# Performance work log

Measured on AMD Instinct MI355X. Metric: run time of the kernel, lower is better.

The kernel has to match this reference:

```python
import jax, jax.numpy as jnp
import numpy as np
from jax import lax

B, H, W, C = 2, 96, 96, 96
D_STATE, D_CONV, EXPAND = 16, 3, 2
D_INNER = EXPAND * C            # 192 (VSSBlock inner width)
DM = D_INNER                    # Mamba d_model; Mamba expand=1 -> mamba d_inner == DM
DT_RANK = -(-DM // 16)          # ceil(192/16) = 12


def setup_inputs() -> dict:
    key = jax.random.key(0)
    ks = jax.random.split(key, 12)
    s = lambda k, shp, sc=0.02: jax.random.normal(k, shp, jnp.float32) * sc
    return {
        "x": jax.random.normal(ks[0], (B, H, W, C), jnp.float32),
        "norm_w": jnp.ones((C,), jnp.float32),
        "norm_b": jnp.zeros((C,), jnp.float32),
        "in_proj_w": s(ks[1], (C, 2 * D_INNER)),
        "conv2d_w": s(ks[2], (D_INNER, 1, D_CONV, D_CONV), 0.1),   # depthwise OIHW
        "m_in_proj_w": s(ks[3], (DM, 2 * DM)),
        "m_conv1d_w": s(ks[4], (DM, 1, D_CONV), 0.1),              # depthwise causal OIL
        "m_conv1d_b": jnp.zeros((DM,), jnp.float32),
        "m_x_proj_w": s(ks[5], (DM, DT_RANK + 2 * D_STATE)),
        "m_dt_proj_w": s(ks[6], (DT_RANK, DM), 0.1),
        "m_dt_proj_b": s(ks[7], (DM,), 0.1),
        "m_A_log": jnp.log(jnp.broadcast_to(
            jnp.arange(1, D_STATE + 1, dtype=jnp.float32), (DM, D_STATE))),
        "m_D": jnp.ones((DM,), jnp.float32),
        "m_out_proj_w": s(ks[8], (DM, DM)),
        "out_proj_w": s(ks[9], (D_INNER, C)),
    }


def _layernorm(x, w, b, eps=1e-5):
    mu = x.mean(-1, keepdims=True)
    var = jnp.mean(jnp.square(x - mu), -1, keepdims=True)
    return (x - mu) * lax.rsqrt(var + eps) * w + b


def _selective_scan(u, delta, A, Bm, Cm, Dv):
    # u, delta: (B,L,D); A: (D,N); Bm, Cm: (B,L,N); Dv: (D,)
    dA = jnp.exp(jnp.einsum('bld,dn->bldn', delta, A))           # (B,L,D,N)
    dBu = jnp.einsum('bld,bln->bldn', delta * u, Bm)             # (B,L,D,N)

    def step(h, inp):
        dA_t, dBu_t, C_t = inp
        h = dA_t * h + dBu_t                                      # (B,D,N)
        y = jnp.einsum('bdn,bn->bd', h, C_t)
        return h, y

    h0 = jnp.zeros((u.shape[0], A.shape[0], A.shape[1]), u.dtype)
    xs = (dA.transpose(1, 0, 2, 3), dBu.transpose(1, 0, 2, 3), Cm.transpose(1, 0, 2))
    _, ys = lax.scan(step, h0, xs)
    return ys.transpose(1, 0, 2) + u * Dv                         # (B,L,D)


def _mamba(seq, m_in_proj_w, m_conv1d_w, m_conv1d_b, m_x_proj_w,
           m_dt_proj_w, m_dt_proj_b, m_A_log, m_D, m_out_proj_w):
    # seq: (B,L,DM)
    xm, z = jnp.split(seq @ m_in_proj_w, 2, axis=-1)
    # causal depthwise conv1d over L
    xc = lax.conv_general_dilated(
        jnp.transpose(xm, (0, 2, 1)), m_conv1d_w, (1,), [(D_CONV - 1, 0)],
        feature_group_count=DM, dimension_numbers=('NCH', 'OIH', 'NCH'))
    xm = jax.nn.silu(jnp.transpose(xc + m_conv1d_b[None, :, None], (0, 2, 1)))
    x_dbl = xm @ m_x_proj_w
    dt, Bm, Cm = jnp.split(x_dbl, [DT_RANK, DT_RANK + D_STATE], axis=-1)
    delta = jax.nn.softplus(dt @ m_dt_proj_w + m_dt_proj_b)
    A = -jnp.exp(m_A_log)
    y = _selective_scan(xm, delta, A, Bm, Cm, m_D)
    return (y * jax.nn.silu(z)) @ m_out_proj_w


def reference(x, norm_w, norm_b, in_proj_w, conv2d_w, m_in_proj_w, m_conv1d_w,
              m_conv1d_b, m_x_proj_w, m_dt_proj_w, m_dt_proj_b, m_A_log, m_D,
              m_out_proj_w, out_proj_w):
    Bsz, Hh, Ww, _ = x.shape
    xn = _layernorm(x, norm_w, norm_b)
    x_in, x_gate = jnp.split(xn @ in_proj_w, 2, axis=-1)          # (B,H,W,D_INNER) x2
    # depthwise 3x3 conv, 'same' padding
    xc = lax.conv_general_dilated(
        jnp.transpose(x_in, (0, 3, 1, 2)), conv2d_w, (1, 1), [(1, 1), (1, 1)],
        feature_group_count=D_INNER, dimension_numbers=('NCHW', 'OIHW', 'NCHW'))
    xc = jax.nn.silu(jnp.transpose(xc, (0, 2, 3, 1)))
    seq = xc.reshape(Bsz, Hh * Ww, D_INNER)
    y = _mamba(seq, m_in_proj_w, m_conv1d_w, m_conv1d_b, m_x_proj_w,
               m_dt_proj_w, m_dt_proj_b, m_A_log, m_D, m_out_proj_w)
    y = y.reshape(Bsz, Hh, Ww, D_INNER) * jax.nn.silu(x_gate)
    return x + y @ out_proj_w
```

## Files before the change

kernel.cpp:

```cpp
#include <hip/hip_runtime.h>

#define DEV_INLINE __device__ __forceinline__

constexpr int BATCH = 2;
constexpr int HH = 96, WW = 96, CC = 96;
constexpr int DI = 192;
constexpr int NS = 16;
constexpr int LSEQ = HH * WW;
constexpr int TT = BATCH * LSEQ;
constexpr int CHUNK = 32;
constexpr int NCHUNK = LSEQ / CHUNK;
constexpr int SUP = 24;
constexpr int NSUP = NCHUNK / SUP;
constexpr int QDN = DI * NS;

typedef __attribute__((ext_vector_type(8))) short bf16x8;
typedef __attribute__((ext_vector_type(4))) float f32x4;

DEV_INLINE float silu_f(float x) { return x / (1.f + __expf(-x)); }
DEV_INLINE float softplus_f(float x) {
  return fmaxf(x, 0.f) + log1pf(__expf(-fabsf(x)));
}
DEV_INLINE ushort f2bf(float f) {
  union { float f; unsigned u; } c; c.f = f;
  unsigned u = c.u + 0x7FFF + ((c.u >> 16) & 1);
  return (ushort)(u >> 16);
}

__global__ __launch_bounds__(256)
void castw_kernel(const float* __restrict__ w0, const float* __restrict__ w1,
                  const float* __restrict__ w2, const float* __restrict__ w3,
                  ushort* __restrict__ t0, ushort* __restrict__ t1,
                  ushort* __restrict__ t2, ushort* __restrict__ t3)
{
  int id = blockIdx.x * 256 + threadIdx.x;
  if (id < 36864) {
    int k = id % 96, n = id / 96;
    t0[id] = f2bf(w0[k * 384 + n]);
  } else if (id < 110592) {
    int j = id - 36864; int k = j % 192, n = j / 192;
    t1[j] = f2bf(w1[k * 384 + n]);
  } else if (id < 147456) {
    int j = id - 110592; int k = j % 192, n = j / 192;
    t2[j] = f2bf(w2[k * 192 + n]);
  } else {
    int j = id - 147456; int k = j % 192, n = j / 192;
    t3[j] = (n < 96) ? f2bf(w3[k * 96 + n]) : (ushort)0;
  }
}

__global__ __launch_bounds__(256)
void ln_kernel(const float* __restrict__ x, const float* __restrict__ w,
               const float* __restrict__ bb, ushort* __restrict__ xn)
{
  int wid = (blockIdx.x * blockDim.x + threadIdx.x) >> 6;
  int lane = threadIdx.x & 63;
  if (wid >= TT) return;
  const float* xr = x + (size_t)wid * CC;
  float v0 = xr[lane];
  float v1 = (lane < 32) ? xr[64 + lane] : 0.f;
  float s = v0 + v1, ss = v0 * v0 + v1 * v1;
#pragma unroll
  for (int off = 32; off >= 1; off >>= 1) {
    s  += __shfl_xor(s, off);
    ss += __shfl_xor(ss, off);
  }
  float mean = s * (1.f / 96.f);
  float var  = ss * (1.f / 96.f) - mean * mean;
  float rstd = rsqrtf(var + 1e-5f);
  ushort* o = xn + (size_t)wid * CC;
  o[lane] = f2bf((v0 - mean) * rstd * w[lane] + bb[lane]);
  if (lane < 32) o[64 + lane] = f2bf((v1 - mean) * rstd * w[64 + lane] + bb[64 + lane]);
}

template<int EPI, int OUTF>
__global__ __launch_bounds__(256)
void mfma_gemm_kernel(const ushort* __restrict__ A, int lda,
                      const ushort* __restrict__ Bt, int ldb,
                      void* __restrict__ Cout, int ldc, int N, int K,
                      const float* __restrict__ aux, int ldaux)
{
  const int tid = threadIdx.x;
  const int wid = tid >> 6, lane = tid & 63;
  const int wm = wid >> 1, wn = wid & 1;
  const int m0 = blockIdx.x * 128 + wm * 64;
  const int n0 = blockIdx.y * 64 + wn * 32;
  const int row16 = lane & 15, quad = lane >> 4;

  f32x4 acc[4][2];
  const f32x4 z4 = {0.f, 0.f, 0.f, 0.f};
#pragma unroll
  for (int i = 0; i < 4; ++i)
#pragma unroll
    for (int j = 0; j < 2; ++j) acc[i][j] = z4;

  for (int k0 = 0; k0 < K; k0 += 32) {
    bf16x8 a[4], b[2];
#pragma unroll
    for (int i = 0; i < 4; ++i)
      a[i] = *(const bf16x8*)(A + (size_t)(m0 + i * 16 + row16) * lda + k0 + quad * 8);
#pragma unroll
    for (int j = 0; j < 2; ++j)
      b[j] = *(const bf16x8*)(Bt + (size_t)(n0 + j * 16 + row16) * ldb + k0 + quad * 8);
#pragma unroll
    for (int i = 0; i < 4; ++i)
#pragma unroll
      for (int j = 0; j < 2; ++j)
        acc[i][j] = __builtin_amdgcn_mfma_f32_16x16x32_bf16(a[i], b[j], acc[i][j], 0, 0, 0);
  }

#pragma unroll
  for (int i = 0; i < 4; ++i) {
    const int rowb = m0 + i * 16 + quad * 4;
#pragma unroll
    for (int j = 0; j < 2; ++j) {
      const int col = n0 + j * 16 + row16;
      if (col < N) {
#pragma unroll
        for (int r = 0; r < 4; ++r) {
          float v = acc[i][j][r];
          const int row = rowb + r;
          if (EPI == 1) v *= silu_f(aux[(size_t)row * ldaux + col]);
          else if (EPI == 2) v += aux[(size_t)row * ldaux + col];
          if (OUTF == 0) ((float*)Cout)[(size_t)row * ldc + col] = v;
          else ((ushort*)Cout)[(size_t)row * ldc + col] = f2bf(v);
        }
      }
    }
  }
}

__global__ __launch_bounds__(256)
void gemm_f32_kernel(const float* __restrict__ A, int lda,
                     const float* __restrict__ B, int ldb,
                     float* __restrict__ C, int ldc, int N, int K)
{
  __shared__ __align__(16) float As[16][132];
  __shared__ __align__(16) float Bs[16][64];
  const int tid = threadIdx.x;
  const int tx = tid & 15;
  const int ty = tid >> 4;
  const int m0 = blockIdx.x * 128;
  const int n0 = blockIdx.y * 64;
  const int arow = tid >> 2;
  const int akq  = (tid & 3) << 2;
  const int brow = tid >> 4;
  const int bcol = (tid & 15) << 2;

  float acc[8][4];
#pragma unroll
  for (int i = 0; i < 8; ++i)
#pragma unroll
    for (int j = 0; j < 4; ++j) acc[i][j] = 0.f;

  for (int k0 = 0; k0 < K; k0 += 16) {
    float4 a0 = *(const float4*)(A + (size_t)(m0 + arow) * lda + (k0 + akq));
    float4 a1 = *(const float4*)(A + (size_t)(m0 + arow + 64) * lda + (k0 + akq));
    float4 bv = make_float4(0.f, 0.f, 0.f, 0.f);
    if (n0 + bcol < N)
      bv = *(const float4*)(B + (size_t)(k0 + brow) * ldb + (n0 + bcol));
    __syncthreads();
    As[akq + 0][arow] = a0.x;
    As[akq + 1][arow] = a0.y;
    As[akq + 2][arow] = a0.z;
    As[akq + 3][arow] = a0.w;
    As[akq + 0][arow + 64] = a1.x;
    As[akq + 1][arow + 64] = a1.y;
    As[akq + 2][arow + 64] = a1.z;
    As[akq + 3][arow + 64] = a1.w;
    *(float4*)&Bs[brow][bcol] = bv;
    __syncthreads();
#pragma unroll
    for (int k = 0; k < 16; ++k) {
      float4 av0 = *(const float4*)&As[k][ty * 8];
      float4 av1 = *(const float4*)&As[k][ty * 8 + 4];
      float4 bv0 = *(const float4*)&Bs[k][tx * 4];
      float am[8] = {av0.x, av0.y, av0.z, av0.w, av1.x, av1.y, av1.z, av1.w};
      float bn[4] = {bv0.x, bv0.y, bv0.z, bv0.w};
#pragma unroll
      for (int i = 0; i < 8; ++i)
#pragma unroll
        for (int j = 0; j < 4; ++j)
          acc[i][j] = fmaf(am[i], bn[j], acc[i][j]);
    }
  }

  const int col = n0 + tx * 4;
  if (col < N) {
#pragma unroll
    for (int i = 0; i < 8; ++i) {
      const int row = m0 + ty * 8 + i;
      *(float4*)(C + (size_t)row * ldc + col) =
          make_float4(acc[i][0], acc[i][1], acc[i][2], acc[i][3]);
    }
  }
}

__global__ __launch_bounds__(256)
void conv2d_silu_kernel(const float* __restrict__ xz0, const float* __restrict__ w,
                        ushort* __restrict__ xc)
{
  __shared__ float ws[DI * 9];
  for (int i = threadIdx.x; i < DI * 9; i += 256) ws[i] = w[i];
  __syncthreads();
  int id = blockIdx.x * 256 + threadIdx.x;
  int dq = id % 48;
  int p  = id / 48;
  int j = p % WW;
  int i = (p / WW) % HH;
  int b = p / (WW * HH);
  int d = dq * 4;
  float a0 = 0.f, a1 = 0.f, a2 = 0.f, a3 = 0.f;
#pragma unroll
  for (int ki = 0; ki < 3; ++ki) {
    int ii = i + ki - 1;
    if (ii < 0 || ii >= HH) continue;
#pragma unroll
    for (int kj = 0; kj < 3; ++kj) {
      int jj = j + kj - 1;
      if (jj < 0 || jj >= WW) continue;
      const float4 v = *(const float4*)(xz0 + ((size_t)((b * HH + ii) * WW + jj)) * 384 + d);
      int wk = ki * 3 + kj;
      a0 = fmaf(v.x, ws[(d + 0) * 9 + wk], a0);
      a1 = fmaf(v.y, ws[(d + 1) * 9 + wk], a1);
      a2 = fmaf(v.z, ws[(d + 2) * 9 + wk], a2);
      a3 = fmaf(v.w, ws[(d + 3) * 9 + wk], a3);
    }
  }
  ushort4 o;
  o.x = f2bf(silu_f(a0)); o.y = f2bf(silu_f(a1));
  o.z = f2bf(silu_f(a2)); o.w = f2bf(silu_f(a3));
  *(ushort4*)(xc + (size_t)p * DI + d) = o;
}

__global__ __launch_bounds__(256)
void conv1d_silu_kernel(const float* __restrict__ xz1, const float* __restrict__ w,
                        const float* __restrict__ bias, float* __restrict__ xm)
{
  int id = blockIdx.x * 256 + threadIdx.x;
  int dq = id % 48;
  int t  = id / 48;
  int l  = t % LSEQ;
  int d  = dq * 4;
  float a0 = bias[d + 0], a1 = bias[d + 1], a2 = bias[d + 2], a3 = bias[d + 3];
#pragma unroll
  for (int k = 0; k < 3; ++k) {
    int ll = l + k - 2;
    if (ll < 0) continue;
    const float4 v = *(const float4*)(xz1 + (size_t)(t + k - 2) * 384 + d);
    a0 = fmaf(v.x, w[(d + 0) * 3 + k], a0);
    a1 = fmaf(v.y, w[(d + 1) * 3 + k], a1);
    a2 = fmaf(v.z, w[(d + 2) * 3 + k], a2);
    a3 = fmaf(v.w, w[(d + 3) * 3 + k], a3);
  }
  float4 o = make_float4(silu_f(a0), silu_f(a1), silu_f(a2), silu_f(a3));
  *(float4*)(xm + (size_t)t * DI + d) = o;
}

__global__ __launch_bounds__(256)
void dtproj_kernel(const float* __restrict__ xdbl, const float* __restrict__ Wdt,
                   const float* __restrict__ bdt, float* __restrict__ delta)
{
  int id = blockIdx.x * 256 + threadIdx.x;
  int d = id % DI;
  int t = id / DI;
  float acc = bdt[d];
#pragma unroll
  for (int r = 0; r < 12; ++r)
    acc = fmaf(xdbl[(size_t)t * 44 + r], Wdt[r * DI + d], acc);
  delta[id] = softplus_f(acc);
}

__global__ __launch_bounds__(192)
void scan1_kernel(const float* __restrict__ dlt, const float* __restrict__ xmb,
                  const float* __restrict__ xdbl, const float* __restrict__ Alog,
                  float* __restrict__ P, float* __restrict__ E)
{
  const int d = threadIdx.x;
  const int g = blockIdx.x % NCHUNK;
  const int b = blockIdx.x / NCHUNK;
  const int t0 = b * LSEQ + g * CHUNK;
  float Av[16];
#pragma unroll
  for (int j = 0; j < 16; ++j) Av[j] = -__expf(Alog[d * 16 + j]);
  float e[16];
#pragma unroll
  for (int j = 0; j < 16; ++j) e[j] = 0.f;
  float sdl = 0.f;
#pragma unroll 2
  for (int l = 0; l < CHUNK; ++l) {
    const int t = t0 + l;
    float dl = dlt[(size_t)t * DI + d];
    float u  = xmb[(size_t)t * DI + d];
    const float4 B0 = *(const float4*)(xdbl + (size_t)t * 44 + 12);
    const float4 B1 = *(const float4*)(xdbl + (size_t)t * 44 + 16);
    const float4 B2 = *(const float4*)(xdbl + (size_t)t * 44 + 20);
    const float4 B3 = *(const float4*)(xdbl + (size_t)t * 44 + 24);
    const float Bv[16] = {B0.x, B0.y, B0.z, B0.w, B1.x, B1.y, B1.z, B1.w,
                          B2.x, B2.y, B2.z, B2.w, B3.x, B3.y, B3.z, B3.w};
    float du = dl * u;
    sdl += dl;
#pragma unroll
    for (int j = 0; j < 16; ++j) {
      float a = __expf(dl * Av[j]);
      e[j] = fmaf(a, e[j], du * Bv[j]);
    }
  }
  size_t base = ((size_t)(b * NCHUNK + g)) * QDN + d * 16;
#pragma unroll
  for (int j = 0; j < 16; ++j) {
    P[base + j] = __expf(Av[j] * sdl);
    E[base + j] = e[j];
  }
}

__global__ __launch_bounds__(256)
void scan2a_kernel(const float* __restrict__ P, const float* __restrict__ E,
                   float* __restrict__ SP, float* __restrict__ SE)
{
  int id = blockIdx.x * 256 + threadIdx.x;
  int q = id % QDN;
  int s = (id / QDN) % NSUP;
  int b = id / (QDN * NSUP);
  float cp = 1.f, ce = 0.f;
#pragma unroll 4
  for (int c = 0; c < SUP; ++c) {
    size_t idx = ((size_t)(b * NCHUNK + s * SUP + c)) * QDN + q;
    float p = P[idx], e = E[idx];
    ce = fmaf(p, ce, e);
    cp *= p;
  }
  SP[id] = cp; SE[id] = ce;
}

__global__ __launch_bounds__(256)
void scan2b_kernel(const float* __restrict__ SP, const float* __restrict__ SE,
                   float* __restrict__ Hsup)
{
  int id = blockIdx.x * 256 + threadIdx.x;
  int q = id % QDN;
  int b = id / QDN;
  float carry = 0.f;
#pragma unroll
  for (int s = 0; s < NSUP; ++s) {
    size_t idx = ((size_t)(b * NSUP + s)) * QDN + q;
    Hsup[idx] = carry;
    carry = fmaf(SP[idx], carry, SE[idx]);
  }
}

__global__ __launch_bounds__(256)
void scan2c_kernel(const float* __restrict__ P, const float* __restrict__ E,
                   const float* __restrict__ Hsup, float* __restrict__ Hin)
{
  int id = blockIdx.x * 256 + threadIdx.x;
  int q = id % QDN;
  int s = (id / QDN) % NSUP;
  int b = id / (QDN * NSUP);
  float h = Hsup[id];
#pragma unroll 4
  for (int c = 0; c < SUP; ++c) {
    size_t idx = ((size_t)(b * NCHUNK + s * SUP + c)) * QDN + q;
    Hin[idx] = h;
    h = fmaf(P[idx], h, E[idx]);
  }
}

__global__ __launch_bounds__(192)
void scan3_kernel(const float* __restrict__ dlt, const float* __restrict__ xmb,
                  const float* __restrict__ xdbl, const float* __restrict__ Alog,
                  const float* __restrict__ Dv, const float* __restrict__ xz1,
                  const float* __restrict__ Hin, ushort* __restrict__ yout)
{
  const int d = threadIdx.x;
  const int g = blockIdx.x % NCHUNK;
  const int b = blockIdx.x / NCHUNK;
  const int t0 = b * LSEQ + g * CHUNK;
  float Av[16];
#pragma unroll
  for (int j = 0; j < 16; ++j) Av[j] = -__expf(Alog[d * 16 + j]);
  const float Dd = Dv[d];
  float h[16];
  {
    size_t hb = ((size_t)(b * NCHUNK + g)) * QDN + d * 16;
#pragma unroll
    for (int j = 0; j < 16; ++j) h[j] = Hin[hb + j];
  }
#pragma unroll 2
  for (int l = 0; l < CHUNK; ++l) {
    const int t = t0 + l;
    float dl = dlt[(size_t)t * DI + d];
    float u  = xmb[(size_t)t * DI + d];
    const float4 B0 = *(const float4*)(xdbl + (size_t)t * 44 + 12);
    const float4 B1 = *(const float4*)(xdbl + (size_t)t * 44 + 16);
    const float4 B2 = *(const float4*)(xdbl + (size_t)t * 44 + 20);
    const float4 B3 = *(const float4*)(xdbl + (size_t)t * 44 + 24);
    const float4 C0 = *(const float4*)(xdbl + (size_t)t * 44 + 28);
    const float4 C1 = *(const float4*)(xdbl + (size_t)t * 44 + 32);
    const float4 C2 = *(const float4*)(xdbl + (size_t)t * 44 + 36);
    const float4 C3 = *(const float4*)(xdbl + (size_t)t * 44 + 40);
    const float Bv[16] = {B0.x, B0.y, B0.z, B0.w, B1.x, B1.y, B1.z, B1.w,
                          B2.x, B2.y, B2.z, B2.w, B3.x, B3.y, B3.z, B3.w};
    const float Cv[16] = {C0.x, C0.y, C0.z, C0.w, C1.x, C1.y, C1.z, C1.w,
                          C2.x, C2.y, C2.z, C2.w, C3.x, C3.y, C3.z, C3.w};
    float du = dl * u;
    float y0 = 0.f, y1 = 0.f, y2 = 0.f, y3 = 0.f;
#pragma unroll
    for (int j = 0; j < 16; ++j) {
      float a = __expf(dl * Av[j]);
      h[j] = fmaf(a, h[j], du * Bv[j]);
      if ((j & 3) == 0) y0 = fmaf(h[j], Cv[j], y0);
      else if ((j & 3) == 1) y1 = fmaf(h[j], Cv[j], y1);
      else if ((j & 3) == 2) y2 = fmaf(h[j], Cv[j], y2);
      else y3 = fmaf(h[j], Cv[j], y3);
    }
    float y = (y0 + y1) + (y2 + y3) + u * Dd;
    float z = xz1[(size_t)t * 384 + 192 + d];
    yout[(size_t)t * DI + d] = f2bf(y * silu_f(z));
  }
}

extern "C" void kernel_launch(void* const* d_in, const int* in_sizes, int n_in,
                              void* d_out, int out_size, void* d_ws, size_t ws_size,
                              hipStream_t stream)
{
  const float* x         = (const float*)d_in[0];
  const float* norm_w    = (const float*)d_in[1];
  const float* norm_b    = (const float*)d_in[2];
  const float* in_proj_w = (const float*)d_in[3];
  const float* conv2d_w  = (const float*)d_in[4];
  const float* m_in_proj = (const float*)d_in[5];
  const float* m_c1d_w   = (const float*)d_in[6];
  const float* m_c1d_b   = (const float*)d_in[7];
  const float* m_x_proj  = (const float*)d_in[8];
  const float* m_dt_w    = (const float*)d_in[9];
  const float* m_dt_b    = (const float*)d_in[10];
  const float* m_A_log   = (const float*)d_in[11];
  const float* m_D       = (const float*)d_in[12];
  const float* m_out_w   = (const float*)d_in[13];
  const float* out_w     = (const float*)d_in[14];
  float* out = (float*)d_out;

  char* wp = (char*)d_ws;
  auto alloc = [&](size_t bytes) {
    char* r = wp; wp += (bytes + 255) & ~(size_t)255; return r;
  };
  ushort* Wt0   = (ushort*)alloc(36864 * 2);
  ushort* Wt1   = (ushort*)alloc(73728 * 2);
  ushort* Wt2   = (ushort*)alloc(36864 * 2);
  ushort* Wt3   = (ushort*)alloc(24576 * 2);
  ushort* xn_bf = (ushort*)alloc((size_t)TT * 96 * 2);
  float*  xz0   = (float*)alloc((size_t)TT * 384 * 4);
  ushort* xc_bf = (ushort*)alloc((size_t)TT * 192 * 2);
  float*  xz1   = (float*)alloc((size_t)TT * 384 * 4);
  float*  xmb   = (float*)alloc((size_t)TT * 192 * 4);
  float*  xdbl  = (float*)alloc((size_t)TT * 44 * 4);
  float*  dlt   = (float*)alloc((size_t)TT * 192 * 4);
  float*  Pb    = (float*)alloc((size_t)BATCH * NCHUNK * QDN * 4);
  float*  Eb    = (float*)alloc((size_t)BATCH * NCHUNK * QDN * 4);
  float*  Hin   = (float*)alloc((size_t)BATCH * NCHUNK * QDN * 4);
  float*  SPb   = (float*)alloc((size_t)BATCH * NSUP * QDN * 4);
  float*  SEb   = (float*)alloc((size_t)BATCH * NSUP * QDN * 4);
  float*  Hsup  = (float*)alloc((size_t)BATCH * NSUP * QDN * 4);
  ushort* yfin  = (ushort*)alloc((size_t)TT * 192 * 2);
  ushort* yg    = (ushort*)alloc((size_t)TT * 192 * 2);

  castw_kernel<<<672, 256, 0, stream>>>(in_proj_w, m_in_proj, m_out_w, out_w,
                                        Wt0, Wt1, Wt2, Wt3);
  ln_kernel<<<TT / 4, 256, 0, stream>>>(x, norm_w, norm_b, xn_bf);
  mfma_gemm_kernel<0, 0><<<dim3(TT / 128, 6), 256, 0, stream>>>(
      xn_bf, 96, Wt0, 96, xz0, 384, 384, 96, nullptr, 0);
  conv2d_silu_kernel<<<TT * 48 / 256, 256, 0, stream>>>(xz0, conv2d_w, xc_bf);
  mfma_gemm_kernel<0, 0><<<dim3(TT / 128, 6), 256, 0, stream>>>(
      xc_bf, 192, Wt1, 192, xz1, 384, 384, 192, nullptr, 0);
  conv1d_silu_kernel<<<TT * 48 / 256, 256, 0, stream>>>(xz1, m_c1d_w, m_c1d_b, xmb);
  gemm_f32_kernel<<<dim3(TT / 128, 1), 256, 0, stream>>>(xmb, 192, m_x_proj, 44, xdbl, 44, 44, 192);
  dtproj_kernel<<<TT * 192 / 256, 256, 0, stream>>>(xdbl, m_dt_w, m_dt_b, dlt);
  scan1_kernel<<<BATCH * NCHUNK, 192, 0, stream>>>(dlt, xmb, xdbl, m_A_log, Pb, Eb);
  scan2a_kernel<<<BATCH * NSUP * QDN / 256, 256, 0, stream>>>(Pb, Eb, SPb, SEb);
  scan2b_kernel<<<BATCH * QDN / 256, 256, 0, stream>>>(SPb, SEb, Hsup);
  scan2c_kernel<<<BATCH * NSUP * QDN / 256, 256, 0, stream>>>(Pb, Eb, Hsup, Hin);
  scan3_kernel<<<BATCH * NCHUNK, 192, 0, stream>>>(dlt, xmb, xdbl, m_A_log, m_D, xz1, Hin, yfin);
  mfma_gemm_kernel<1, 1><<<dim3(TT / 128, 3), 256, 0, stream>>>(
      yfin, 192, Wt2, 192, yg, 192, 192, 192, xz0 + 192, 384);
  mfma_gemm_kernel<2, 0><<<dim3(TT / 128, 2), 256, 0, stream>>>(
      yg, 192, Wt3, 192, out, 96, 96, 192, x, 96);
}
```

Baseline: 271.0 us.

## Fuse conv1d, x_proj and dt_proj into one MFMA kernel; store intermediates in bf16

Replaces the separate conv1d+silu, fp32 x_proj GEMM and dt_proj kernels with a single mamba_prep kernel. It computes the causal conv into shared memory, then runs x_proj and dt_proj as bf16 MFMA, with B/C reordered into a compact 32-float layout. The in_proj intermediates xz0/xz1 and xm are now stored as bf16. The GEMM epilogue is transposed so each lane writes four contiguous outputs per token. The aim is to cut launches and global memory traffic, at the cost of reduced precision in dt, B and C and in the activations feeding the scan.

Result: no change. 267.6 us (-1.3%).

```diff
diff --git a/kernel.cpp b/kernel.cpp
--- a/kernel.cpp
+++ b/kernel.cpp
@@ -26,12 +26,17 @@
   unsigned u = c.u + 0x7FFF + ((c.u >> 16) & 1);
   return (ushort)(u >> 16);
 }
+DEV_INLINE float bf2f(ushort u) {
+  union { unsigned u; float f; } c; c.u = ((unsigned)u) << 16; return c.f;
+}
 
 __global__ __launch_bounds__(256)
 void castw_kernel(const float* __restrict__ w0, const float* __restrict__ w1,
                   const float* __restrict__ w2, const float* __restrict__ w3,
+                  const float* __restrict__ wx, const float* __restrict__ wdt,
                   ushort* __restrict__ t0, ushort* __restrict__ t1,
-                  ushort* __restrict__ t2, ushort* __restrict__ t3)
+                  ushort* __restrict__ t2, ushort* __restrict__ t3,
+                  ushort* __restrict__ t4, ushort* __restrict__ t5)
 {
   int id = blockIdx.x * 256 + threadIdx.x;
   if (id < 36864) {
@@ -43,9 +48,19 @@
   } else if (id < 147456) {
     int j = id - 110592; int k = j % 192, n = j / 192;
     t2[j] = f2bf(w2[k * 192 + n]);
-  } else {
+  } else if (id < 172032) {
     int j = id - 147456; int k = j % 192, n = j / 192;
     t3[j] = (n < 96) ? f2bf(w3[k * 96 + n]) : (ushort)0;
+  } else if (id < 181248) {
+    int j = id - 172032; int k = j % 192, n = j / 192;
+    float v = 0.f;
+    if (n < 16) v = wx[k * 44 + 12 + n];
+    else if (n < 32) v = wx[k * 44 + 28 + (n - 16)];
+    else if (n < 44) v = wx[k * 44 + (n - 32)];
+    t4[j] = f2bf(v);
+  } else {
+    int j = id - 181248; int r = j % 32, d = j / 32;
+    t5[j] = (r < 12) ? f2bf(wdt[r * 192 + d]) : (ushort)0;
   }
 }
 
@@ -78,14 +93,14 @@
 void mfma_gemm_kernel(const ushort* __restrict__ A, int lda,
                       const ushort* __restrict__ Bt, int ldb,
                       void* __restrict__ Cout, int ldc, int N, int K,
-                      const float* __restrict__ aux, int ldaux)
+                      const void* __restrict__ aux, int ldaux)
 {
   const int tid = threadIdx.x;
   const int wid = tid >> 6, lane = tid & 63;
   const int wm = wid >> 1, wn = wid & 1;
   const int m0 = blockIdx.x * 128 + wm * 64;
   const int n0 = blockIdx.y * 64 + wn * 32;
-  const int row16 = lane & 15, quad = lane >> 4;
+  const int l16 = lane & 15, quad = lane >> 4;
 
   f32x4 acc[4][2];
   const f32x4 z4 = {0.f, 0.f, 0.f, 0.f};
@@ -95,109 +110,52 @@
     for (int j = 0; j < 2; ++j) acc[i][j] = z4;
 
   for (int k0 = 0; k0 < K; k0 += 32) {
-    bf16x8 a[4], b[2];
+    bf16x8 xf[4], wf[2];
 #pragma unroll
     for (int i = 0; i < 4; ++i)
-      a[i] = *(const bf16x8*)(A + (size_t)(m0 + i * 16 + row16) * lda + k0 + quad * 8);
+      xf[i] = *(const bf16x8*)(A + (size_t)(m0 + i * 16 + l16) * lda + k0 + quad * 8);
 #pragma unroll
     for (int j = 0; j < 2; ++j)
-      b[j] = *(const bf16x8*)(Bt + (size_t)(n0 + j * 16 + row16) * ldb + k0 + quad * 8);
+      wf[j] = *(const bf16x8*)(Bt + (size_t)(n0 + j * 16 + l16) * ldb + k0 + quad * 8);
 #pragma unroll
     for (int i = 0; i < 4; ++i)
 #pragma unroll
       for (int j = 0; j < 2; ++j)
-        acc[i][j] = __builtin_amdgcn_mfma_f32_16x16x32_bf16(a[i], b[j], acc[i][j], 0, 0, 0);
+        acc[i][j] = __builtin_amdgcn_mfma_f32_16x16x32_bf16(wf[j], xf[i], acc[i][j], 0, 0, 0);
   }
 
 #pragma unroll
   for (int i = 0; i < 4; ++i) {
-    const int rowb = m0 + i * 16 + quad * 4;
+    const int token = m0 + i * 16 + l16;
 #pragma unroll
     for (int j = 0; j < 2; ++j) {
-      const int col = n0 + j * 16 + row16;
-      if (col < N) {
-#pragma unroll
-        for (int r = 0; r < 4; ++r) {
-          float v = acc[i][j][r];
-          const int row = rowb + r;
-          if (EPI == 1) v *= silu_f(aux[(size_t)row * ldaux + col]);
-          else if (EPI == 2) v += aux[(size_t)row * ldaux + col];
-          if (OUTF == 0) ((float*)Cout)[(size_t)row * ldc + col] = v;
-          else ((ushort*)Cout)[(size_t)row * ldc + col] = f2bf(v);
-        }
+      const int nb = n0 + j * 16 + quad * 4;
+      if (nb >= N) continue;
+      float v[4];
+#pragma unroll
+      for (int r = 0; r < 4; ++r) v[r] = acc[i][j][r];
+      if (EPI == 1) {
+        const ushort4 g4 = *(const ushort4*)((const ushort*)aux + (size_t)token * ldaux + nb);
+        v[0] *= silu_f(bf2f(g4.x)); v[1] *= silu_f(bf2f(g4.y));
+        v[2] *= silu_f(bf2f(g4.z)); v[3] *= silu_f(bf2f(g4.w));
+      } else if (EPI == 2) {
+        const float4 r4 = *(const float4*)((const float*)aux + (size_t)token * ldaux + nb);
+        v[0] += r4.x; v[1] += r4.y; v[2] += r4.z; v[3] += r4.w;
       }
-    }
-  }
-}
-
-__global__ __launch_bounds__(256)
-void gemm_f32_kernel(const float* __restrict__ A, int lda,
-                     const float* __restrict__ B, int ldb,
-                     float* __restrict__ C, int ldc, int N, int K)
-{
-  __shared__ __align__(16) float As[16][132];
-  __shared__ __align__(16) float Bs[16][64];
-  const int tid = threadIdx.x;
-  const int tx = tid & 15;
-  const int ty = tid >> 4;
-  const int m0 = blockIdx.x * 128;
-  const int n0 = blockIdx.y * 64;
-  const int arow = tid >> 2;
-  const int akq  = (tid & 3) << 2;
-  const int brow = tid >> 4;
-  const int bcol = (tid & 15) << 2;
-
-  float acc[8][4];
-#pragma unroll
-  for (int i = 0; i < 8; ++i)
-#pragma unroll
-    for (int j = 0; j < 4; ++j) acc[i][j] = 0.f;
-
-  for (int k0 = 0; k0 < K; k0 += 16) {
-    float4 a0 = *(const float4*)(A + (size_t)(m0 + arow) * lda + (k0 + akq));
-    float4 a1 = *(const float4*)(A + (size_t)(m0 + arow + 64) * lda + (k0 + akq));
-    float4 bv = make_float4(0.f, 0.f, 0.f, 0.f);
-    if (n0 + bcol < N)
-      bv = *(const float4*)(B + (size_t)(k0 + brow) * ldb + (n0 + bcol));
-    __syncthreads();
-    As[akq + 0][arow] = a0.x;
-    As[akq + 1][arow] = a0.y;
-    As[akq + 2][arow] = a0.z;
-    As[akq + 3][arow] = a0.w;
-    As[akq + 0][arow + 64] = a1.x;
-    As[akq + 1][arow + 64] = a1.y;
-    As[akq + 2][arow + 64] = a1.z;
-    As[akq + 3][arow + 64] = a1.w;
-    *(float4*)&Bs[brow][bcol] = bv;
-    __syncthreads();
-#pragma unroll
-    for (int k = 0; k < 16; ++k) {
-      float4 av0 = *(const float4*)&As[k][ty * 8];
-      float4 av1 = *(const float4*)&As[k][ty * 8 + 4];
-      float4 bv0 = *(const float4*)&Bs[k][tx * 4];
-      float am[8] = {av0.x, av0.y, av0.z, av0.w, av1.x, av1.y, av1.z, av1.w};
-      float bn[4] = {bv0.x, bv0.y, bv0.z, bv0.w};
-#pragma unroll
-      for (int i = 0; i < 8; ++i)
-#pragma unroll
-        for (int j = 0; j < 4; ++j)
-          acc[i][j] = fmaf(am[i], bn[j], acc[i][j]);
-    }
-  }
-
-  const int col = n0 + tx * 4;
-  if (col < N) {
-#pragma unroll
-    for (int i = 0; i < 8; ++i) {
-      const int row = m0 + ty * 8 + i;
-      *(float4*)(C + (size_t)row * ldc + col) =
-          make_float4(acc[i][0], acc[i][1], acc[i][2], acc[i][3]);
-    }
-  }
-}
-
-__global__ __launch_bounds__(256)
-void conv2d_silu_kernel(const float* __restrict__ xz0, const float* __restrict__ w,
+      if (OUTF == 0) {
+        *(float4*)((float*)Cout + (size_t)token * ldc + nb) =
+            make_float4(v[0], v[1], v[2], v[3]);
+      } else {
+        ushort4 o;
+        o.x = f2bf(v[0]); o.y = f2bf(v[1]); o.z = f2bf(v[2]); o.w = f2bf(v[3]);
+        *(ushort4*)((ushort*)Cout + (size_t)token * ldc + nb) = o;
+      }
+    }
+  }
+}
+
+__global__ __launch_bounds__(256)
+void conv2d_silu_kernel(const ushort* __restrict__ xz0, const float* __restrict__ w,
                         ushort* __restrict__ xc)
 {
   __shared__ float ws[DI * 9];
@@ -219,12 +177,12 @@
     for (int kj = 0; kj < 3; ++kj) {
       int jj = j + kj - 1;
       if (jj < 0 || jj >= WW) continue;
-      const float4 v = *(const float4*)(xz0 + ((size_t)((b * HH + ii) * WW + jj)) * 384 + d);
+      const ushort4 v = *(const ushort4*)(xz0 + ((size_t)((b * HH + ii) * WW + jj)) * 384 + d);
       int wk = ki * 3 + kj;
-      a0 = fmaf(v.x, ws[(d + 0) * 9 + wk], a0);
-      a1 = fmaf(v.y, ws[(d + 1) * 9 + wk], a1);
-      a2 = fmaf(v.z, ws[(d + 2) * 9 + wk], a2);
-      a3 = fmaf(v.w, ws[(d + 3) * 9 + wk], a3);
+      a0 = fmaf(bf2f(v.x), ws[(d + 0) * 9 + wk], a0);
+      a1 = fmaf(bf2f(v.y), ws[(d + 1) * 9 + wk], a1);
+      a2 = fmaf(bf2f(v.z), ws[(d + 2) * 9 + wk], a2);
+      a3 = fmaf(bf2f(v.w), ws[(d + 3) * 9 + wk], a3);
     }
   }
   ushort4 o;
@@ -234,46 +192,93 @@
 }
 
 __global__ __launch_bounds__(256)
-void conv1d_silu_kernel(const float* __restrict__ xz1, const float* __restrict__ w,
-                        const float* __restrict__ bias, float* __restrict__ xm)
-{
-  int id = blockIdx.x * 256 + threadIdx.x;
-  int dq = id % 48;
-  int t  = id / 48;
-  int l  = t % LSEQ;
-  int d  = dq * 4;
-  float a0 = bias[d + 0], a1 = bias[d + 1], a2 = bias[d + 2], a3 = bias[d + 3];
-#pragma unroll
-  for (int k = 0; k < 3; ++k) {
-    int ll = l + k - 2;
-    if (ll < 0) continue;
-    const float4 v = *(const float4*)(xz1 + (size_t)(t + k - 2) * 384 + d);
-    a0 = fmaf(v.x, w[(d + 0) * 3 + k], a0);
-    a1 = fmaf(v.y, w[(d + 1) * 3 + k], a1);
-    a2 = fmaf(v.z, w[(d + 2) * 3 + k], a2);
-    a3 = fmaf(v.w, w[(d + 3) * 3 + k], a3);
-  }
-  float4 o = make_float4(silu_f(a0), silu_f(a1), silu_f(a2), silu_f(a3));
-  *(float4*)(xm + (size_t)t * DI + d) = o;
-}
-
-__global__ __launch_bounds__(256)
-void dtproj_kernel(const float* __restrict__ xdbl, const float* __restrict__ Wdt,
-                   const float* __restrict__ bdt, float* __restrict__ delta)
-{
-  int id = blockIdx.x * 256 + threadIdx.x;
-  int d = id % DI;
-  int t = id / DI;
-  float acc = bdt[d];
-#pragma unroll
-  for (int r = 0; r < 12; ++r)
-    acc = fmaf(xdbl[(size_t)t * 44 + r], Wdt[r * DI + d], acc);
-  delta[id] = softplus_f(acc);
+void mamba_prep_kernel(const ushort* __restrict__ xz1, const float* __restrict__ cw,
+                       const float* __restrict__ cb, const ushort* __restrict__ Wxt,
+                       const ushort* __restrict__ Wdtt, const float* __restrict__ bdt,
+                       ushort* __restrict__ xmb_bf, float* __restrict__ xdbl_bc,
+                       float* __restrict__ dlt)
+{
+  __shared__ ushort sxm[64][200];
+  __shared__ ushort sdtb[64][40];
+  const int tid = threadIdx.x;
+  const int t0 = blockIdx.x * 64;
+  const int l0 = t0 % LSEQ;
+
+  for (int i = tid; i < 64 * 40 / 2; i += 256) ((unsigned*)sdtb)[i] = 0;
+
+#pragma unroll
+  for (int it = 0; it < 12; ++it) {
+    int task = tid + it * 256;
+    int dq = task % 48, tl = task / 48;
+    int d = dq * 4;
+    int t = t0 + tl, l = l0 + tl;
+    float a0 = cb[d], a1 = cb[d + 1], a2 = cb[d + 2], a3 = cb[d + 3];
+#pragma unroll
+    for (int k = 0; k < 3; ++k) {
+      if (l + k - 2 < 0) continue;
+      const ushort4 v = *(const ushort4*)(xz1 + (size_t)(t + k - 2) * 384 + d);
+      a0 = fmaf(bf2f(v.x), cw[(d + 0) * 3 + k], a0);
+      a1 = fmaf(bf2f(v.y), cw[(d + 1) * 3 + k], a1);
+      a2 = fmaf(bf2f(v.z), cw[(d + 2) * 3 + k], a2);
+      a3 = fmaf(bf2f(v.w), cw[(d + 3) * 3 + k], a3);
+    }
+    ushort4 o;
+    o.x = f2bf(silu_f(a0)); o.y = f2bf(silu_f(a1));
+    o.z = f2bf(silu_f(a2)); o.w = f2bf(silu_f(a3));
+    *(ushort4*)&sxm[tl][d] = o;
+    *(ushort4*)(xmb_bf + (size_t)t * DI + d) = o;
+  }
+  __syncthreads();
+
+  const int wid = tid >> 6, lane = tid & 63;
+  const int l16 = lane & 15, quad = lane >> 4;
+  const int ts = wid * 16;
+  const int token = t0 + ts + l16;
+  const f32x4 z4 = {0.f, 0.f, 0.f, 0.f};
+
+  f32x4 acc1[3] = {z4, z4, z4};
+  for (int k0 = 0; k0 < 192; k0 += 32) {
+    bf16x8 xf = *(const bf16x8*)&sxm[ts + l16][k0 + quad * 8];
+#pragma unroll
+    for (int j = 0; j < 3; ++j) {
+      bf16x8 wf = *(const bf16x8*)(Wxt + (size_t)(j * 16 + l16) * 192 + k0 + quad * 8);
+      acc1[j] = __builtin_amdgcn_mfma_f32_16x16x32_bf16(wf, xf, acc1[j], 0, 0, 0);
+    }
+  }
+#pragma unroll
+  for (int j = 0; j < 2; ++j)
+    *(float4*)(xdbl_bc + (size_t)token * 32 + j * 16 + quad * 4) =
+        make_float4(acc1[j][0], acc1[j][1], acc1[j][2], acc1[j][3]);
+  if (quad < 3) {
+    ushort4 o;
+    o.x = f2bf(acc1[2][0]); o.y = f2bf(acc1[2][1]);
+    o.z = f2bf(acc1[2][2]); o.w = f2bf(acc1[2][3]);
+    *(ushort4*)&sdtb[ts + l16][quad * 4] = o;
+  }
+  __syncthreads();
+
+  bf16x8 dtf = *(const bf16x8*)&sdtb[ts + l16][quad * 8];
+  f32x4 acc2[12];
+#pragma unroll
+  for (int jj = 0; jj < 12; ++jj) {
+    bf16x8 wf = *(const bf16x8*)(Wdtt + (size_t)(jj * 16 + l16) * 32 + quad * 8);
+    acc2[jj] = __builtin_amdgcn_mfma_f32_16x16x32_bf16(wf, dtf, z4, 0, 0, 0);
+  }
+#pragma unroll
+  for (int jj = 0; jj < 12; ++jj) {
+    const int nb = jj * 16 + quad * 4;
+    float4 dv;
+    dv.x = softplus_f(acc2[jj][0] + bdt[nb + 0]);
+    dv.y = softplus_f(acc2[jj][1] + bdt[nb + 1]);
+    dv.z = softplus_f(acc2[jj][2] + bdt[nb + 2]);
+    dv.w = softplus_f(acc2[jj][3] + bdt[nb + 3]);
+    *(float4*)(dlt + (size_t)token * DI + nb) = dv;
+  }
 }
 
 __global__ __launch_bounds__(192)
-void scan1_kernel(const float* __restrict__ dlt, const float* __restrict__ xmb,
-                  const float* __restrict__ xdbl, const float* __restrict__ Alog,
+void scan1_kernel(const float* __restrict__ dlt, const ushort* __restrict__ xmb,
+                  const float* __restrict__ xdbl_bc, const float* __restrict__ Alog,
                   float* __restrict__ P, float* __restrict__ E)
 {
   const int d = threadIdx.x;
@@ -291,11 +296,11 @@
   for (int l = 0; l < CHUNK; ++l) {
     const int t = t0 + l;
     float dl = dlt[(size_t)t * DI + d];
-    float u  = xmb[(size_t)t * DI + d];
-    const float4 B0 = *(const float4*)(xdbl + (size_t)t * 44 + 12);
-    const float4 B1 = *(const float4*)(xdbl + (size_t)t * 44 + 16);
-    const float4 B2 = *(const float4*)(xdbl + (size_t)t * 44 + 20);
-    const float4 B3 = *(const float4*)(xdbl + (size_t)t * 44 + 24);
+    float u  = bf2f(xmb[(size_t)t * DI + d]);
+    const float4 B0 = *(const float4*)(xdbl_bc + (size_t)t * 32 + 0);
+    const float4 B1 = *(const float4*)(xdbl_bc + (size_t)t * 32 + 4);
+    const float4 B2 = *(const float4*)(xdbl_bc + (size_t)t * 32 + 8);
+    const float4 B3 = *(const float4*)(xdbl_bc + (size_t)t * 32 + 12);
     const float Bv[16] = {B0.x, B0.y, B0.z, B0.w, B1.x, B1.y, B1.z, B1.w,
                           B2.x, B2.y, B2.z, B2.w, B3.x, B3.y, B3.z, B3.w};
     float du = dl * u;
@@ -367,9 +372,9 @@
 }
 
 __global__ __launch_bounds__(192)
-void scan3_kernel(const float* __restrict__ dlt, const float* __restrict__ xmb,
-                  const float* __restrict__ xdbl, const float* __restrict__ Alog,
-                  const float* __restrict__ Dv, const float* __restrict__ xz1,
+void scan3_kernel(const float* __restrict__ dlt, const ushort* __restrict__ xmb,
+                  const float* __restrict__ xdbl_bc, const float* __restrict__ Alog,
+                  const float* __restrict__ Dv, const ushort* __restrict__ xz1,
                   const float* __restrict__ Hin, ushort* __restrict__ yout)
 {
   const int d = threadIdx.x;
@@ -390,15 +395,15 @@
   for (int l = 0; l < CHUNK; ++l) {
     const int t = t0 + l;
     float dl = dlt[(size_t)t * DI + d];
-    float u  = xmb[(size_t)t * DI + d];
-    const float4 B0 = *(const float4*)(xdbl + (size_t)t * 44 + 12);
-    const float4 B1 = *(const float4*)(xdbl + (size_t)t * 44 + 16);
-    const float4 B2 = *(const float4*)(xdbl + (size_t)t * 44 + 20);
-    const float4 B3 = *(const float4*)(xdbl + (size_t)t * 44 + 24);
-    const float4 C0 = *(const float4*)(xdbl + (size_t)t * 44 + 28);
-    const float4 C1 = *(const float4*)(xdbl + (size_t)t * 44 + 32);
-    const float4 C2 = *(const float4*)(xdbl + (size_t)t * 44 + 36);
-    const float4 C3 = *(const float4*)(xdbl + (size_t)t * 44 + 40);
+    float u  = bf2f(xmb[(size_t)t * DI + d]);
+    const float4 B0 = *(const float4*)(xdbl_bc + (size_t)t * 32 + 0);
+    const float4 B1 = *(const float4*)(xdbl_bc + (size_t)t * 32 + 4);
+    const float4 B2 = *(const float4*)(xdbl_bc + (size_t)t * 32 + 8);
+    const float4 B3 = *(const float4*)(xdbl_bc + (size_t)t * 32 + 12);
+    const float4 C0 = *(const float4*)(xdbl_bc + (size_t)t * 32 + 16);
+    const float4 C1 = *(const float4*)(xdbl_bc + (size_t)t * 32 + 20);
+    const float4 C2 = *(const float4*)(xdbl_bc + (size_t)t * 32 + 24);
+    const float4 C3 = *(const float4*)(xdbl_bc + (size_t)t * 32 + 28);
     const float Bv[16] = {B0.x, B0.y, B0.z, B0.w, B1.x, B1.y, B1.z, B1.w,
                           B2.x, B2.y, B2.z, B2.w, B3.x, B3.y, B3.z, B3.w};
     const float Cv[16] = {C0.x, C0.y, C0.z, C0.w, C1.x, C1.y, C1.z, C1.w,
@@ -415,7 +420,7 @@
       else y3 = fmaf(h[j], Cv[j], y3);
     }
     float y = (y0 + y1) + (y2 + y3) + u * Dd;
-    float z = xz1[(size_t)t * 384 + 192 + d];
+    float z = bf2f(xz1[(size_t)t * 384 + 192 + d]);
     yout[(size_t)t * DI + d] = f2bf(y * silu_f(z));
   }
 }
@@ -445,42 +450,44 @@
   auto alloc = [&](size_t bytes) {
     char* r = wp; wp += (bytes + 255) & ~(size_t)255; return r;
   };
-  ushort* Wt0   = (ushort*)alloc(36864 * 2);
-  ushort* Wt1   = (ushort*)alloc(73728 * 2);
-  ushort* Wt2   = (ushort*)alloc(36864 * 2);
-  ushort* Wt3   = (ushort*)alloc(24576 * 2);
-  ushort* xn_bf = (ushort*)alloc((size_t)TT * 96 * 2);
-  float*  xz0   = (float*)alloc((size_t)TT * 384 * 4);
-  ushort* xc_bf = (ushort*)alloc((size_t)TT * 192 * 2);
-  float*  xz1   = (float*)alloc((size_t)TT * 384 * 4);
-  float*  xmb   = (float*)alloc((size_t)TT * 192 * 4);
-  float*  xdbl  = (float*)alloc((size_t)TT * 44 * 4);
-  float*  dlt   = (float*)alloc((size_t)TT * 192 * 4);
-  float*  Pb    = (float*)alloc((size_t)BATCH * NCHUNK * QDN * 4);
-  float*  Eb    = (float*)alloc((size_t)BATCH * NCHUNK * QDN * 4);
-  float*  Hin   = (float*)alloc((size_t)BATCH * NCHUNK * QDN * 4);
-  float*  SPb   = (float*)alloc((size_t)BATCH * NSUP * QDN * 4);
-  float*  SEb   = (float*)alloc((size_t)BATCH * NSUP * QDN * 4);
-  float*  Hsup  = (float*)alloc((size_t)BATCH * NSUP * QDN * 4);
-  ushort* yfin  = (ushort*)alloc((size_t)TT * 192 * 2);
-  ushort* yg    = (ushort*)alloc((size_t)TT * 192 * 2);
-
-  castw_kernel<<<672, 256, 0, stream>>>(in_proj_w, m_in_proj, m_out_w, out_w,
-                                        Wt0, Wt1, Wt2, Wt3);
+  ushort* Wt0    = (ushort*)alloc(36864 * 2);
+  ushort* Wt1    = (ushort*)alloc(73728 * 2);
+  ushort* Wt2    = (ushort*)alloc(36864 * 2);
+  ushort* Wt3    = (ushort*)alloc(24576 * 2);
+  ushort* Wxt    = (ushort*)alloc(9216 * 2);
+  ushort* Wdtt   = (ushort*)alloc(6144 * 2);
+  ushort* xn_bf  = (ushort*)alloc((size_t)TT * 96 * 2);
+  ushort* xz0    = (ushort*)alloc((size_t)TT * 384 * 2);
+  ushort* xc_bf  = (ushort*)alloc((size_t)TT * 192 * 2);
+  ushort* xz1    = (ushort*)alloc((size_t)TT * 384 * 2);
+  ushort* xmb_bf = (ushort*)alloc((size_t)TT * 192 * 2);
+  float*  xdbl_bc= (float*)alloc((size_t)TT * 32 * 4);
+  float*  dlt    = (float*)alloc((size_t)TT * 192 * 4);
+  float*  Pb     = (float*)alloc((size_t)BATCH * NCHUNK * QDN * 4);
+  float*  Eb     = (float*)alloc((size_t)BATCH * NCHUNK * QDN * 4);
+  float*  Hin    = (float*)alloc((size_t)BATCH * NCHUNK * QDN * 4);
+  float*  SPb    = (float*)alloc((size_t)BATCH * NSUP * QDN * 4);
+  float*  SEb    = (float*)alloc((size_t)BATCH * NSUP * QDN * 4);
+  float*  Hsup   = (float*)alloc((size_t)BATCH * NSUP * QDN * 4);
+  ushort* yfin   = (ushort*)alloc((size_t)TT * 192 * 2);
+  ushort* yg     = (ushort*)alloc((size_t)TT * 192 * 2);
+
+  castw_kernel<<<732, 256, 0, stream>>>(in_proj_w, m_in_proj, m_out_w, out_w,
+                                        m_x_proj, m_dt_w,
+                                        Wt0, Wt1, Wt2, Wt3, Wxt, Wdtt);
   ln_kernel<<<TT / 4, 256, 0, stream>>>(x, norm_w, norm_b, xn_bf);
-  mfma_gemm_kernel<0, 0><<<dim3(TT / 128, 6), 256, 0, stream>>>(
+  mfma_gemm_kernel<0, 1><<<dim3(TT / 128, 6), 256, 0, stream>>>(
       xn_bf, 96, Wt0, 96, xz0, 384, 384, 96, nullptr, 0);
   conv2d_silu_kernel<<<TT * 48 / 256, 256, 0, stream>>>(xz0, conv2d_w, xc_bf);
-  mfma_gemm_kernel<0, 0><<<dim3(TT / 128, 6), 256, 0, stream>>>(
+  mfma_gemm_kernel<0, 1><<<dim3(TT / 128, 6), 256, 0, stream>>>(
       xc_bf, 192, Wt1, 192, xz1, 384, 384, 192, nullptr, 0);
-  conv1d_silu_kernel<<<TT * 48 / 256, 256, 0, stream>>>(xz1, m_c1d_w, m_c1d_b, xmb);
-  gemm_f32_kernel<<<dim3(TT / 128, 1), 256, 0, stream>>>(xmb, 192, m_x_proj, 44, xdbl, 44, 44, 192);
-  dtproj_kernel<<<TT * 192 / 256, 256, 0, stream>>>(xdbl, m_dt_w, m_dt_b, dlt);
-  scan1_kernel<<<BATCH * NCHUNK, 192, 0, stream>>>(dlt, xmb, xdbl, m_A_log, Pb, Eb);
+  mamba_prep_kernel<<<TT / 64, 256, 0, stream>>>(
+      xz1, m_c1d_w, m_c1d_b, Wxt, Wdtt, m_dt_b, xmb_bf, xdbl_bc, dlt);
+  scan1_kernel<<<BATCH * NCHUNK, 192, 0, stream>>>(dlt, xmb_bf, xdbl_bc, m_A_log, Pb, Eb);
   scan2a_kernel<<<BATCH * NSUP * QDN / 256, 256, 0, stream>>>(Pb, Eb, SPb, SEb);
   scan2b_kernel<<<BATCH * QDN / 256, 256, 0, stream>>>(SPb, SEb, Hsup);
   scan2c_kernel<<<BATCH * NSUP * QDN / 256, 256, 0, stream>>>(Pb, Eb, Hsup, Hin);
-  scan3_kernel<<<BATCH * NCHUNK, 192, 0, stream>>>(dlt, xmb, xdbl, m_A_log, m_D, xz1, Hin, yfin);
+  scan3_kernel<<<BATCH * NCHUNK, 192, 0, stream>>>(dlt, xmb_bf, xdbl_bc, m_A_log, m_D, xz1, Hin, yfin);
   mfma_gemm_kernel<1, 1><<<dim3(TT / 128, 3), 256, 0, stream>>>(
       yfin, 192, Wt2, 192, yg, 192, 192, 192, xz0 + 192, 384);
   mfma_gemm_kernel<2, 0><<<dim3(TT / 128, 2), 256, 0, stream>>>(
```
